# Optimization experiments

Measured on AMD Instinct MI355X. Metric: run time of the kernel, lower is better.

## Reference

```python
import jax, jax.numpy as jnp
import numpy as np

DIM = 256
HEADS = 8
DIM_HEAD = 64
SLICE_NUM = 64
INNER = HEADS * DIM_HEAD
B, N = 4, 32768


def setup_inputs() -> dict:
    key = jax.random.key(0)
    ks = jax.random.split(key, 12)
    s_in = 1.0 / np.sqrt(DIM)
    s_h = 1.0 / np.sqrt(DIM_HEAD)
    s_o = 1.0 / np.sqrt(INNER)
    return {
        "x": jax.random.normal(ks[0], (B, N, DIM), dtype=jnp.float32),
        "Wfx": jax.random.normal(ks[1], (INNER, DIM), dtype=jnp.float32) * s_in,
        "bfx": jax.random.normal(ks[2], (INNER,), dtype=jnp.float32) * 0.01,
        "Wx": jax.random.normal(ks[3], (INNER, DIM), dtype=jnp.float32) * s_in,
        "bx": jax.random.normal(ks[4], (INNER,), dtype=jnp.float32) * 0.01,
        "Wslice": jax.random.normal(ks[5], (SLICE_NUM, DIM_HEAD), dtype=jnp.float32) * s_h,
        "bslice": jax.random.normal(ks[6], (SLICE_NUM,), dtype=jnp.float32) * 0.01,
        "temperature": jnp.ones((1, HEADS, 1, 1), dtype=jnp.float32) * 0.5,
        "Wq": jax.random.normal(ks[7], (DIM_HEAD, DIM_HEAD), dtype=jnp.float32) * s_h,
        "Wk": jax.random.normal(ks[8], (DIM_HEAD, DIM_HEAD), dtype=jnp.float32) * s_h,
        "Wv": jax.random.normal(ks[9], (DIM_HEAD, DIM_HEAD), dtype=jnp.float32) * s_h,
        "Wout": jax.random.normal(ks[10], (DIM, INNER), dtype=jnp.float32) * s_o,
        "bout": jax.random.normal(ks[11], (DIM,), dtype=jnp.float32) * 0.01,
    }


def reference(x, Wfx, bfx, Wx, bx, Wslice, bslice, temperature, Wq, Wk, Wv, Wout, bout):
    b, n, c = x.shape
    Ch = Wq.shape[0]
    H = Wfx.shape[0] // Ch
    # project and split heads: [B, H, N, Ch]
    fx_mid = (x @ Wfx.T + bfx).reshape(b, n, H, Ch).transpose(0, 2, 1, 3)
    x_mid = (x @ Wx.T + bx).reshape(b, n, H, Ch).transpose(0, 2, 1, 3)
    # soft slice assignment: [B, H, N, M]
    temp = jnp.clip(temperature, 0.1, 5.0)
    logits = (x_mid @ Wslice.T + bslice) / temp
    sw = jax.nn.softmax(logits, axis=-1)
    sw = sw / (sw.sum(axis=2, keepdims=True) + 1e-5)  # normalize over N per slice
    # slice tokens: [B, H, M, Ch]
    slice_token = jnp.einsum('bhnc,bhng->bhgc', fx_mid, sw)
    # attention over slices
    q = slice_token @ Wq.T
    k = slice_token @ Wk.T
    v = slice_token @ Wv.T
    scale = Ch ** (-0.5)
    attn = jax.nn.softmax(jnp.einsum('bhgc,bhmc->bhgm', q, k) * scale, axis=-1)
    out_tok = attn @ v  # [B, H, M, Ch]
    # deslice back to N points
    out_x = jnp.einsum('bhgc,bhng->bhnc', out_tok, sw)
    out_x = out_x.transpose(0, 2, 1, 3).reshape(b, n, H * Ch)
    return out_x @ Wout.T + bout
```

## Files before the change

### kernel.cpp

```cpp
#include <hip/hip_runtime.h>
#include <hip/hip_bf16.h>

typedef __attribute__((ext_vector_type(8))) short bf16x8;
typedef __attribute__((ext_vector_type(4))) float f32x4;

union U16 { int4 v; ushort u[8]; };

__device__ __forceinline__ float b2f(ushort u){ return __uint_as_float(((unsigned int)u)<<16); }
__device__ __forceinline__ ushort f2b(float f){ return __bfloat16_as_ushort(__float2bfloat16(f)); }
__device__ __forceinline__ f32x4 mfma16(bf16x8 a, bf16x8 b, f32x4 c){
  return __builtin_amdgcn_mfma_f32_16x16x32_bf16(a,b,c,0,0,0);
}

__global__ void k_prep(const float* __restrict__ Wfx, const float* __restrict__ bfx,
                       const float* __restrict__ Wx,  const float* __restrict__ bx,
                       const float* __restrict__ Wout, const float* __restrict__ Wsl,
                       ushort* __restrict__ Wcat, float* __restrict__ bcat,
                       ushort* __restrict__ Wo16, ushort* __restrict__ Wsl16){
  int i = blockIdx.x*256 + threadIdx.x;
  if (i < 131072) Wcat[i] = f2b(Wfx[i]);
  else if (i < 262144) Wcat[i] = f2b(Wx[i-131072]);
  if (i < 131072) Wo16[i] = f2b(Wout[i]);
  if (i < 4096) Wsl16[i] = f2b(Wsl[i]);
  if (i < 512) bcat[i] = bfx[i];
  else if (i < 1024) bcat[i] = bx[i-512];
}

__global__ void k_zero(float* __restrict__ p, int n){
  int i = blockIdx.x*256 + threadIdx.x;
  if (i < n) p[i] = 0.f;
}

__global__ __launch_bounds__(256,2) void k_proj(
    const float* __restrict__ x, const ushort* __restrict__ Wcat,
    const float* __restrict__ bcat, ushort* __restrict__ fx, ushort* __restrict__ xm){
  __shared__ ushort lA[64*264];
  const int t = threadIdx.x;
  const long tok0 = (long)blockIdx.x*64;
  {
    const int r4 = t>>6, c4 = t&63;
    for (int i=0;i<16;i++){
      const int row = i*4 + r4;
      float4 v = *(const float4*)&x[(size_t)(tok0+row)*256 + c4*4];
      ushort4 hv; hv.x=f2b(v.x); hv.y=f2b(v.y); hv.z=f2b(v.z); hv.w=f2b(v.w);
      *(ushort4*)&lA[row*264 + c4*4] = hv;
    }
  }
  __syncthreads();
  const int w=t>>6, l=t&63, l16=l&15, q8=l>>4;
  const int j0 = blockIdx.y*256 + w*64;
  f32x4 acc[4][4] = {};
  #pragma unroll 2
  for (int ks=0; ks<8; ks++){
    bf16x8 af[4], bfg[4];
    for (int i=0;i<4;i++) af[i] = *(const bf16x8*)&lA[(i*16+l16)*264 + ks*32 + q8*8];
    for (int j=0;j<4;j++) bfg[j] = *(const bf16x8*)&Wcat[(size_t)(j0+j*16+l16)*256 + ks*32 + q8*8];
    for (int i=0;i<4;i++)
      for (int j=0;j<4;j++)
        acc[i][j] = mfma16(af[i], bfg[j], acc[i][j]);
  }
  for (int j=0;j<4;j++){
    const int col = j0 + j*16 + l16;
    const float bc = bcat[col];
    ushort* dst = (col<512) ? fx : xm;
    const int cc = (col<512) ? col : col-512;
    for (int i=0;i<4;i++)
      for (int r=0;r<4;r++)
        dst[(size_t)(tok0 + i*16 + q8*4 + r)*512 + cc] = f2b(acc[i][j][r] + bc);
  }
}

__global__ __launch_bounds__(256,4) void k_slice(
    const ushort* __restrict__ xm, const ushort* __restrict__ Wsl16,
    const float* __restrict__ bslv, const float* __restrict__ temp,
    ushort* __restrict__ swn, float* __restrict__ cs){
  __shared__ float lcs[512];
  const int t = threadIdx.x, w=t>>6, l=t&63, l16=l&15, q8=l>>4;
  const long tok0 = (long)blockIdx.x*64;
  const int b = (int)(tok0 >> 15);
  for (int i=t;i<512;i+=256) lcs[i]=0.f;
  bf16x8 bw[4][2];
  for (int j=0;j<4;j++)
    for (int ks=0;ks<2;ks++)
      bw[j][ks] = *(const bf16x8*)&Wsl16[(j*16+l16)*64 + ks*32 + q8*8];
  float bj[4];
  for (int j=0;j<4;j++) bj[j] = bslv[j*16+l16];
  float itemp[8];
  for (int h=0;h<8;h++){
    float tp = temp[h]; tp = fminf(fmaxf(tp,0.1f),5.0f); itemp[h] = 1.0f/tp;
  }
  __syncthreads();
  const size_t rowbase = (size_t)(tok0 + w*16 + l16)*512;
  for (int h=0;h<8;h++){
    bf16x8 af0 = *(const bf16x8*)&xm[rowbase + h*64 + q8*8];
    bf16x8 af1 = *(const bf16x8*)&xm[rowbase + h*64 + 32 + q8*8];
    f32x4 acc[4] = {};
    for (int j=0;j<4;j++) acc[j] = mfma16(af0, bw[j][0], acc[j]);
    for (int j=0;j<4;j++) acc[j] = mfma16(af1, bw[j][1], acc[j]);
    const float it = itemp[h];
    float csum[4] = {0.f,0.f,0.f,0.f};
    for (int r=0;r<4;r++){
      float v[4]; float m = -1e30f;
      for (int j=0;j<4;j++){ v[j] = (acc[j][r] + bj[j])*it; m = fmaxf(m, v[j]); }
      for (int mk=1;mk<16;mk<<=1) m = fmaxf(m, __shfl_xor(m, mk, 64));
      float s = 0.f;
      for (int j=0;j<4;j++){ v[j] = __expf(v[j]-m); s += v[j]; }
      for (int mk=1;mk<16;mk<<=1) s += __shfl_xor(s, mk, 64);
      const float inv = 1.0f/s;
      const long tok = tok0 + w*16 + q8*4 + r;
      ushort* dst = &swn[((size_t)tok*8 + h)*64];
      for (int j=0;j<4;j++){
        float q = b2f(f2b(v[j]*inv));
        csum[j] += q;
        dst[j*16+l16] = f2b(q);
      }
    }
    for (int j=0;j<4;j++){
      float v = csum[j];
      v += __shfl_xor(v, 16, 64);
      v += __shfl_xor(v, 32, 64);
      if (q8==0) atomicAdd(&lcs[h*64 + j*16 + l16], v);
    }
  }
  __syncthreads();
  for (int i=t;i<512;i+=256) atomicAdd(&cs[(size_t)b*512 + i], lcs[i]);
}

__global__ __launch_bounds__(256,2) void k_accum(
    const ushort* __restrict__ swn, const ushort* __restrict__ fx,
    float* __restrict__ sraw){
  __shared__ ushort lW[64*136];
  __shared__ ushort lF[64*136];
  const int t = threadIdx.x;
  const int bh = blockIdx.y, b = bh>>3, h = bh&7;
  const long tokb = (long)b*32768 + (long)blockIdx.x*512;
  const int w=t>>6, l=t&63, l16=l&15, q8=l>>4;
  const int nr = t>>3, g8 = (t&7)*8;
  f32x4 acc[4] = {};
  for (int sub=0; sub<4; sub++){
    __syncthreads();
    for (int ri=0; ri<4; ri++){
      const int nl = ri*32 + nr;
      const long tok = tokb + sub*128 + nl;
      U16 sv; sv.v = *(const int4*)&swn[((size_t)tok*8 + h)*64 + g8];
      U16 fv; fv.v = *(const int4*)&fx[(size_t)tok*512 + h*64 + g8];
      for (int j=0;j<8;j++){
        lW[(g8+j)*136 + nl] = sv.u[j];
        lF[(g8+j)*136 + nl] = fv.u[j];
      }
    }
    __syncthreads();
    #pragma unroll
    for (int kk=0; kk<4; kk++){
      bf16x8 af = *(const bf16x8*)&lW[(w*16+l16)*136 + kk*32 + q8*8];
      for (int j=0;j<4;j++){
        bf16x8 bfg = *(const bf16x8*)&lF[(j*16+l16)*136 + kk*32 + q8*8];
        acc[j] = mfma16(af, bfg, acc[j]);
      }
    }
  }
  for (int j=0;j<4;j++)
    for (int r=0;r<4;r++)
      atomicAdd(&sraw[((size_t)bh*64 + w*16 + q8*4 + r)*64 + j*16 + l16], acc[j][r]);
}

__global__ __launch_bounds__(256,1) void k_attn(
    const float* __restrict__ sraw, const float* __restrict__ cs,
    const float* __restrict__ Wq, const float* __restrict__ Wk, const float* __restrict__ Wv,
    ushort* __restrict__ ott){
  __shared__ float st[64*68], t1[64*68], t2[64*68];
  __shared__ ushort tw[64*68];
  __shared__ float pmax[256], psum[256], csl[64];
  const int t = threadIdx.x, bh = blockIdx.x;
  if (t < 64) csl[t] = 1.0f/(cs[bh*64+t] + 1e-5f);
  __syncthreads();
  for (int i=0;i<16;i++){ int idx=i*256+t; st[(idx>>6)*68+(idx&63)] = sraw[(size_t)bh*4096+idx]*csl[idx>>6]; }
  for (int i=0;i<16;i++){ int idx=i*256+t; tw[(idx>>6)*68+(idx&63)] = f2b(Wq[idx]); }
  __syncthreads();
  const int w=t>>6, lane=t&63;
  float o[16];
  #define GT(OUT) do{ for(int j=0;j<16;j++) OUT[j]=0.f; \
    for(int c4=0;c4<16;c4++){ float4 xv=*(float4*)&st[lane*68+c4*4]; \
      for(int j=0;j<16;j++){ ushort4 wv=*(const ushort4*)&tw[(w*16+j)*68+c4*4]; \
        OUT[j]+=xv.x*b2f(wv.x)+xv.y*b2f(wv.y)+xv.z*b2f(wv.z)+xv.w*b2f(wv.w);} } }while(0)
  GT(o);
  __syncthreads();
  for (int j=0;j<16;j++) t1[lane*68 + w*16+j] = o[j];
  for (int i=0;i<16;i++){ int idx=i*256+t; tw[(idx>>6)*68+(idx&63)] = f2b(Wk[idx]); }
  __syncthreads();
  GT(o);
  __syncthreads();
  for (int j=0;j<16;j++) t2[lane*68 + w*16+j] = o[j];
  __syncthreads();
  float sc[16];
  for (int j=0;j<16;j++) sc[j]=0.f;
  for (int c4=0;c4<16;c4++){
    float4 qv = *(float4*)&t1[lane*68+c4*4];
    for (int j=0;j<16;j++){
      float4 kv = *(float4*)&t2[(w*16+j)*68+c4*4];
      sc[j] += qv.x*kv.x + qv.y*kv.y + qv.z*kv.z + qv.w*kv.w;
    }
  }
  float pm = -1e30f;
  for (int j=0;j<16;j++){ sc[j]*=0.125f; pm=fmaxf(pm,sc[j]); }
  pmax[lane*4+w]=pm; __syncthreads();
  const float m = fmaxf(fmaxf(pmax[lane*4+0],pmax[lane*4+1]),fmaxf(pmax[lane*4+2],pmax[lane*4+3]));
  float s=0.f;
  for (int j=0;j<16;j++){ sc[j]=__expf(sc[j]-m); s+=sc[j]; }
  psum[lane*4+w]=s; __syncthreads();
  const float inv = 1.0f/(psum[lane*4+0]+psum[lane*4+1]+psum[lane*4+2]+psum[lane*4+3]);
  for (int j=0;j<16;j++) t1[lane*68 + w*16+j] = sc[j]*inv;
  for (int i=0;i<16;i++){ int idx=i*256+t; tw[(idx>>6)*68+(idx&63)] = f2b(Wv[idx]); }
  __syncthreads();
  GT(o);
  __syncthreads();
  for (int j=0;j<16;j++) t2[lane*68 + w*16+j] = o[j];
  __syncthreads();
  float ot[16];
  for (int j=0;j<16;j++) ot[j]=0.f;
  for (int m4=0;m4<16;m4++){
    float4 av = *(float4*)&t1[lane*68+m4*4];
    for (int j=0;j<16;j++){
      int c = w*16+j;
      ot[j] += av.x*t2[(m4*4+0)*68+c] + av.y*t2[(m4*4+1)*68+c]
             + av.z*t2[(m4*4+2)*68+c] + av.w*t2[(m4*4+3)*68+c];
    }
  }
  const float ics = csl[lane];
  for (int j=0;j<16;j++)
    ott[(size_t)bh*4096 + (size_t)(w*16+j)*64 + lane] = f2b(ot[j]*ics);
  #undef GT
}

__global__ __launch_bounds__(256,2) void k_deslice(
    const ushort* __restrict__ swn, const ushort* __restrict__ ott,
    ushort* __restrict__ ox){
  __shared__ ushort lS[32*520];
  const int t = threadIdx.x;
  const long tok0 = (long)blockIdx.x*32;
  const int b = (int)(tok0 >> 15);
  const int rw = t>>3, sg = t&7;
  for (int i=0;i<8;i++)
    *(int4*)&lS[rw*520 + i*64 + sg*8] = *(const int4*)&swn[(size_t)(tok0+rw)*512 + i*64 + sg*8];
  __syncthreads();
  const int w=t>>6, l=t&63, l16=l&15, q8=l>>4;
  for (int h=0; h<8; h++){
    const int bh = b*8 + h;
    f32x4 acc[2] = {};
    for (int kb=0; kb<2; kb++){
      bf16x8 bfg = *(const bf16x8*)&ott[(size_t)(bh*64 + w*16 + l16)*64 + kb*32 + q8*8];
      for (int i=0;i<2;i++){
        bf16x8 af = *(const bf16x8*)&lS[(i*16+l16)*520 + h*64 + kb*32 + q8*8];
        acc[i] = mfma16(af, bfg, acc[i]);
      }
    }
    for (int i=0;i<2;i++)
      for (int r=0;r<4;r++)
        ox[(size_t)(tok0 + i*16 + q8*4 + r)*512 + h*64 + w*16 + l16] = f2b(acc[i][r]);
  }
}

__global__ __launch_bounds__(256,2) void k_out(
    const ushort* __restrict__ ox, const ushort* __restrict__ Wo16,
    const float* __restrict__ bout, float* __restrict__ out){
  __shared__ ushort lA[32*520];
  const int t = threadIdx.x;
  const long tok0 = (long)blockIdx.x*32;
  const int rw = t>>3, sg = t&7;
  for (int i=0;i<8;i++)
    *(int4*)&lA[rw*520 + i*64 + sg*8] = *(const int4*)&ox[(size_t)(tok0+rw)*512 + i*64 + sg*8];
  __syncthreads();
  const int w=t>>6, l=t&63, l16=l&15, q8=l>>4;
  const int j0 = w*64;
  f32x4 acc[2][4] = {};
  #pragma unroll 2
  for (int ks=0; ks<16; ks++){
    bf16x8 af[2], bfg[4];
    for (int i=0;i<2;i++) af[i] = *(const bf16x8*)&lA[(i*16+l16)*520 + ks*32 + q8*8];
    for (int j=0;j<4;j++) bfg[j] = *(const bf16x8*)&Wo16[(size_t)(j0+j*16+l16)*512 + ks*32 + q8*8];
    for (int i=0;i<2;i++)
      for (int j=0;j<4;j++)
        acc[i][j] = mfma16(af[i], bfg[j], acc[i][j]);
  }
  for (int j=0;j<4;j++){
    const int col = j0 + j*16 + l16;
    const float bc = bout[col];
    for (int i=0;i<2;i++)
      for (int r=0;r<4;r++)
        out[(size_t)(tok0 + i*16 + q8*4 + r)*256 + col] = acc[i][j][r] + bc;
  }
}

extern "C" void kernel_launch(void* const* d_in, const int* in_sizes, int n_in,
                              void* d_out, int out_size, void* d_ws, size_t ws_size,
                              hipStream_t stream) {
  (void)in_sizes; (void)n_in; (void)out_size;
  const float* x    = (const float*)d_in[0];
  const float* Wfx  = (const float*)d_in[1];
  const float* bfx  = (const float*)d_in[2];
  const float* Wx   = (const float*)d_in[3];
  const float* bx   = (const float*)d_in[4];
  const float* Wsl  = (const float*)d_in[5];
  const float* bsl  = (const float*)d_in[6];
  const float* temp = (const float*)d_in[7];
  const float* Wq   = (const float*)d_in[8];
  const float* Wk   = (const float*)d_in[9];
  const float* Wv   = (const float*)d_in[10];
  const float* Wout = (const float*)d_in[11];
  const float* bout = (const float*)d_in[12];
  float* out = (float*)d_out;
  char* ws = (char*)d_ws;

  constexpr size_t O_FX   = 0;
  constexpr size_t O_XM   = 134217728;
  constexpr size_t O_SWN  = 268435456;
  constexpr size_t O_SRAW = 402653184;
  constexpr size_t O_CS   = O_SRAW + 524288;
  constexpr size_t O_OTT  = O_CS + 8192;
  constexpr size_t O_WCAT = O_OTT + 262144;
  constexpr size_t O_BCAT = O_WCAT + 524288;
  constexpr size_t O_WOUT = O_BCAT + 4096;
  constexpr size_t O_WSL  = O_WOUT + 262144;
  constexpr size_t NEED   = O_WSL + 8192;
  if (ws_size < NEED) return;

  ushort* fxb  = (ushort*)(ws + O_FX);
  ushort* xmb  = (ushort*)(ws + O_XM);
  ushort* swn  = (ushort*)(ws + O_SWN);
  float*  sraw = (float*)(ws + O_SRAW);
  float*  cs   = (float*)(ws + O_CS);
  ushort* ott  = (ushort*)(ws + O_OTT);
  ushort* Wcat = (ushort*)(ws + O_WCAT);
  float*  bcat = (float*)(ws + O_BCAT);
  ushort* Wo16 = (ushort*)(ws + O_WOUT);
  ushort* Wsl16= (ushort*)(ws + O_WSL);
  ushort* oxb  = xmb;

  k_prep<<<1024,256,0,stream>>>(Wfx,bfx,Wx,bx,Wout,Wsl,Wcat,bcat,Wo16,Wsl16);
  k_zero<<<520,256,0,stream>>>(sraw, 133120);
  k_proj<<<dim3(2048,4),256,0,stream>>>(x,Wcat,bcat,fxb,xmb);
  k_slice<<<2048,256,0,stream>>>(xmb,Wsl16,bsl,temp,swn,cs);
  k_accum<<<dim3(64,32),256,0,stream>>>(swn,fxb,sraw);
  k_attn<<<32,256,0,stream>>>(sraw,cs,Wq,Wk,Wv,ott);
  k_deslice<<<4096,256,0,stream>>>(swn,ott,oxb);
  k_out<<<4096,256,0,stream>>>(oxb,Wo16,bout,out);
}
```

Baseline: 827.1 us.

## Pre-convert x to bf16 and double-buffer token tiles in projection kernel

Adds a separate kernel that converts x to bf16 once, into the swn workspace region before swn is written. The projection kernel no longer reloads and reconverts fp32 x in each of its four column-block launches. Each projection block now handles four 64-token tiles and prefetches the next tile into registers during the MFMA work, with occupancy raised to 3. The accumulate kernel also processes twice as many tokens per block, which halves its grid and the number of atomic flushes. The cost is an extra launch plus a write and read of a bf16 copy of x, and more registers per projection block.

```diff
diff --git a/kernel.cpp b/kernel.cpp
--- a/kernel.cpp
+++ b/kernel.cpp
@@ -31,42 +31,63 @@
   if (i < n) p[i] = 0.f;
 }
 
-__global__ __launch_bounds__(256,2) void k_proj(
-    const float* __restrict__ x, const ushort* __restrict__ Wcat,
+__global__ void k_xcvt(const float* __restrict__ x, ushort* __restrict__ xb){
+  const size_t i = ((size_t)blockIdx.x*256 + threadIdx.x)*8;
+  float4 a = *(const float4*)&x[i];
+  float4 b = *(const float4*)&x[i+4];
+  U16 o;
+  o.u[0]=f2b(a.x); o.u[1]=f2b(a.y); o.u[2]=f2b(a.z); o.u[3]=f2b(a.w);
+  o.u[4]=f2b(b.x); o.u[5]=f2b(b.y); o.u[6]=f2b(b.z); o.u[7]=f2b(b.w);
+  *(int4*)&xb[i] = o.v;
+}
+
+__global__ __launch_bounds__(256,3) void k_proj(
+    const ushort* __restrict__ xb, const ushort* __restrict__ Wcat,
     const float* __restrict__ bcat, ushort* __restrict__ fx, ushort* __restrict__ xm){
   __shared__ ushort lA[64*264];
   const int t = threadIdx.x;
-  const long tok0 = (long)blockIdx.x*64;
-  {
-    const int r4 = t>>6, c4 = t&63;
-    for (int i=0;i<16;i++){
-      const int row = i*4 + r4;
-      float4 v = *(const float4*)&x[(size_t)(tok0+row)*256 + c4*4];
-      ushort4 hv; hv.x=f2b(v.x); hv.y=f2b(v.y); hv.z=f2b(v.z); hv.w=f2b(v.w);
-      *(ushort4*)&lA[row*264 + c4*4] = hv;
-    }
-  }
-  __syncthreads();
   const int w=t>>6, l=t&63, l16=l&15, q8=l>>4;
   const int j0 = blockIdx.y*256 + w*64;
-  f32x4 acc[4][4] = {};
-  #pragma unroll 2
-  for (int ks=0; ks<8; ks++){
-    bf16x8 af[4], bfg[4];
-    for (int i=0;i<4;i++) af[i] = *(const bf16x8*)&lA[(i*16+l16)*264 + ks*32 + q8*8];
-    for (int j=0;j<4;j++) bfg[j] = *(const bf16x8*)&Wcat[(size_t)(j0+j*16+l16)*256 + ks*32 + q8*8];
-    for (int i=0;i<4;i++)
-      for (int j=0;j<4;j++)
-        acc[i][j] = mfma16(af[i], bfg[j], acc[i][j]);
-  }
-  for (int j=0;j<4;j++){
-    const int col = j0 + j*16 + l16;
-    const float bc = bcat[col];
-    ushort* dst = (col<512) ? fx : xm;
-    const int cc = (col<512) ? col : col-512;
-    for (int i=0;i<4;i++)
-      for (int r=0;r<4;r++)
-        dst[(size_t)(tok0 + i*16 + q8*4 + r)*512 + cc] = f2b(acc[i][j][r] + bc);
+  const int srow = t>>5, scol = (t&31)*8;
+  const long tokbase = (long)blockIdx.x*256;
+  int4 stg[8];
+  for (int i=0;i<8;i++)
+    stg[i] = *(const int4*)&xb[(size_t)(tokbase + i*8 + srow)*256 + scol];
+  for (int i=0;i<8;i++)
+    *(int4*)&lA[(i*8+srow)*264 + scol] = stg[i];
+  __syncthreads();
+  for (int tt=0; tt<4; tt++){
+    const long tok0 = tokbase + tt*64;
+    if (tt<3){
+      const long nt = tok0 + 64;
+      for (int i=0;i<8;i++)
+        stg[i] = *(const int4*)&xb[(size_t)(nt + i*8 + srow)*256 + scol];
+    }
+    f32x4 acc[4][4] = {};
+    #pragma unroll 2
+    for (int ks=0; ks<8; ks++){
+      bf16x8 af[4], bfg[4];
+      for (int i=0;i<4;i++) af[i] = *(const bf16x8*)&lA[(i*16+l16)*264 + ks*32 + q8*8];
+      for (int j=0;j<4;j++) bfg[j] = *(const bf16x8*)&Wcat[(size_t)(j0+j*16+l16)*256 + ks*32 + q8*8];
+      for (int i=0;i<4;i++)
+        for (int j=0;j<4;j++)
+          acc[i][j] = mfma16(af[i], bfg[j], acc[i][j]);
+    }
+    for (int j=0;j<4;j++){
+      const int col = j0 + j*16 + l16;
+      const float bc = bcat[col];
+      ushort* dst = (col<512) ? fx : xm;
+      const int cc = (col<512) ? col : col-512;
+      for (int i=0;i<4;i++)
+        for (int r=0;r<4;r++)
+          dst[(size_t)(tok0 + i*16 + q8*4 + r)*512 + cc] = f2b(acc[i][j][r] + bc);
+    }
+    if (tt<3){
+      __syncthreads();
+      for (int i=0;i<8;i++)
+        *(int4*)&lA[(i*8+srow)*264 + scol] = stg[i];
+      __syncthreads();
+    }
   }
 }
 
@@ -133,11 +154,11 @@
   __shared__ ushort lF[64*136];
   const int t = threadIdx.x;
   const int bh = blockIdx.y, b = bh>>3, h = bh&7;
-  const long tokb = (long)b*32768 + (long)blockIdx.x*512;
+  const long tokb = (long)b*32768 + (long)blockIdx.x*1024;
   const int w=t>>6, l=t&63, l16=l&15, q8=l>>4;
   const int nr = t>>3, g8 = (t&7)*8;
   f32x4 acc[4] = {};
-  for (int sub=0; sub<4; sub++){
+  for (int sub=0; sub<8; sub++){
     __syncthreads();
     for (int ri=0; ri<4; ri++){
       const int nl = ri*32 + nr;
@@ -327,6 +348,7 @@
   ushort* fxb  = (ushort*)(ws + O_FX);
   ushort* xmb  = (ushort*)(ws + O_XM);
   ushort* swn  = (ushort*)(ws + O_SWN);
+  ushort* xb   = (ushort*)(ws + O_SWN);
   float*  sraw = (float*)(ws + O_SRAW);
   float*  cs   = (float*)(ws + O_CS);
   ushort* ott  = (ushort*)(ws + O_OTT);
@@ -338,9 +360,10 @@
 
   k_prep<<<1024,256,0,stream>>>(Wfx,bfx,Wx,bx,Wout,Wsl,Wcat,bcat,Wo16,Wsl16);
   k_zero<<<520,256,0,stream>>>(sraw, 133120);
-  k_proj<<<dim3(2048,4),256,0,stream>>>(x,Wcat,bcat,fxb,xmb);
+  k_xcvt<<<16384,256,0,stream>>>(x,xb);
+  k_proj<<<dim3(512,4),256,0,stream>>>(xb,Wcat,bcat,fxb,xmb);
   k_slice<<<2048,256,0,stream>>>(xmb,Wsl16,bsl,temp,swn,cs);
-  k_accum<<<dim3(64,32),256,0,stream>>>(swn,fxb,sraw);
+  k_accum<<<dim3(32,32),256,0,stream>>>(swn,fxb,sraw);
   k_attn<<<32,256,0,stream>>>(sraw,cs,Wq,Wk,Wv,ott);
   k_deslice<<<4096,256,0,stream>>>(swn,ott,oxb);
   k_out<<<4096,256,0,stream>>>(oxb,Wo16,bout,out);
```

New measurement: 870.7 us. 1.05x slower.
